# Kernel optimization log

Hardware: AMD Instinct MI355X
Metric: run time of the kernel (lower is better)

## Reference

```python
import jax, jax.numpy as jnp
import numpy as np

OHKM_K = 8
STRUCT_WEIGHT = 1.0
# Standard COCO person skeleton (19 edges over 17 keypoints)
COCO_PERSON_SKELETON = np.array([
    (15, 13), (13, 11), (16, 14), (14, 12), (11, 12), (5, 11), (6, 12),
    (5, 6), (5, 7), (6, 8), (7, 9), (8, 10), (1, 2), (0, 1), (0, 2),
    (1, 3), (2, 4), (3, 5), (4, 6)], dtype=np.int32)


def setup_inputs() -> dict:
    key = jax.random.key(0)
    k1, k2, k3, k4, k5 = jax.random.split(key, 5)
    B, K, C_paf, H, W = 32, 17, 38, 128, 128
    return {
        "heatmap_pred": jax.random.normal(k1, (B, K, H, W), dtype=jnp.float32),
        "paf_pred": jax.random.normal(k2, (B, C_paf, H, W), dtype=jnp.float32),
        "heatmap_gt": jax.random.uniform(k3, (B, K, H, W), dtype=jnp.float32),
        "paf_gt": jax.random.normal(k4, (B, C_paf, H, W), dtype=jnp.float32),
        "joint_coords_gt": jax.random.randint(k5, (B, K, 2), 0, 128, dtype=jnp.int32),
    }


def _struct_loss(heatmap_pred, joint_coords_gt):
    # pred coords from heatmap argmax (vectorized replacement of the python loop)
    B, K, H, W = heatmap_pred.shape
    idx = jnp.argmax(heatmap_pred.reshape(B, K, H * W), axis=2)  # [B,K]
    px = (idx % W).astype(jnp.float32)
    py = (idx // W).astype(jnp.float32)
    pred = jnp.stack([px, py], axis=-1)                 # [B,K,2] (x,y)
    gt = joint_coords_gt.astype(jnp.float32)            # [B,K,2]
    edges = jnp.asarray(COCO_PERSON_SKELETON)           # [E,2]
    a, b = edges[:, 0], edges[:, 1]
    pred_len = jnp.sqrt(jnp.sum((pred[:, a] - pred[:, b]) ** 2, axis=-1))  # [B,E]
    gt_len = jnp.sqrt(jnp.sum((gt[:, a] - gt[:, b]) ** 2, axis=-1))        # [B,E]
    E = edges.shape[0]  # count: all edges valid
    per_batch = jnp.sum((pred_len - gt_len) ** 2, axis=1) / (E + 1e-6)
    return jnp.mean(per_batch)


def reference(heatmap_pred, paf_pred, heatmap_gt, paf_gt, joint_coords_gt):
    # OHKM heatmap loss: per-keypoint MSE, top-k hardest per sample, mean
    per_kp_loss = jnp.mean((heatmap_pred - heatmap_gt) ** 2, axis=(2, 3))  # [B,K]
    Kk = min(OHKM_K, per_kp_loss.shape[1])
    topk_vals, _ = jax.lax.top_k(per_kp_loss, Kk)                          # [B,Kk]
    heatmap_loss = jnp.mean(jnp.mean(topk_vals, axis=1))
    paf_loss = jnp.mean((paf_pred - paf_gt) ** 2)
    total = heatmap_loss + paf_loss
    total = total + STRUCT_WEIGHT * _struct_loss(heatmap_pred, joint_coords_gt)
    return total
```

## Files before the change

kernel.cpp:

```cpp
#include <hip/hip_runtime.h>
#include <math.h>

#define B_ 32
#define K_ 17
#define H_ 128
#define W_ 128
#define HW_ (H_ * W_)
#define C_PAF_ 38
#define NE_ 19
#define HM_TILES (B_ * K_)
#define HM_BLOCKS (HM_TILES * 2)
#define HM_HALF 8192
#define PAF_BLOCKS 2432
#define THREADS 256
#define PAF_N ((size_t)B_ * C_PAF_ * H_ * W_)
#define PAF_N4 (PAF_N / 4)

typedef float fvec4 __attribute__((ext_vector_type(4)));

__constant__ int c_edge_a[NE_] = {15,13,16,14,11, 5, 6, 5, 5, 6, 7, 8, 1, 0, 0, 1, 2, 3, 4};
__constant__ int c_edge_b[NE_] = {13,11,14,12,12,11,12, 6, 7, 8, 9,10, 2, 1, 2, 3, 4, 5, 6};

#define WS_SSQH 0
#define WS_MH   (HM_BLOCKS)
#define WS_MIH  (2 * HM_BLOCKS)
#define WS_PAF  (3 * HM_BLOCKS)

__global__ __launch_bounds__(THREADS, 8) void pose_reduce_kernel(
    const float* __restrict__ hm_pred, const float* __restrict__ hm_gt,
    const float* __restrict__ paf_pred, const float* __restrict__ paf_gt,
    float* __restrict__ ws_f, int* __restrict__ ws_i)
{
    __shared__ float s_val[4];
    __shared__ float s_ssq[4];
    __shared__ int   s_idx[4];

    const int t = threadIdx.x;
    const int bid = blockIdx.x;
    const int wave = t >> 6;
    const int lane = t & 63;

    if (bid < HM_BLOCKS) {
        const int tile = bid >> 1;
        const int half = bid & 1;
        const size_t off = (size_t)tile * HW_ + (size_t)half * HM_HALF;
        const fvec4* __restrict__ p = (const fvec4*)(hm_pred + off);
        const fvec4* __restrict__ g = (const fvec4*)(hm_gt   + off);
        float ssq[2] = {0.0f, 0.0f};
        float m[2] = {-INFINITY, -INFINITY};
        int mi[2] = {0, 0};
        #pragma unroll
        for (int ob = 0; ob < 4; ++ob) {
            const int v0 = t + (ob * 2 + 0) * THREADS;
            const int v1 = t + (ob * 2 + 1) * THREADS;
            const fvec4 a0 = __builtin_nontemporal_load(p + v0);
            const fvec4 b0 = __builtin_nontemporal_load(g + v0);
            const fvec4 a1 = __builtin_nontemporal_load(p + v1);
            const fvec4 b1 = __builtin_nontemporal_load(g + v1);
            {
                const float d0 = a0.x - b0.x, d1 = a0.y - b0.y;
                const float d2 = a0.z - b0.z, d3 = a0.w - b0.w;
                ssq[0] += d0 * d0 + d1 * d1 + d2 * d2 + d3 * d3;
                float m4 = a0.x; int k4 = 0;
                if (a0.y > m4) { m4 = a0.y; k4 = 1; }
                if (a0.z > m4) { m4 = a0.z; k4 = 2; }
                if (a0.w > m4) { m4 = a0.w; k4 = 3; }
                if (m4 > m[0]) { m[0] = m4; mi[0] = 4 * v0 + k4; }
            }
            {
                const float d0 = a1.x - b1.x, d1 = a1.y - b1.y;
                const float d2 = a1.z - b1.z, d3 = a1.w - b1.w;
                ssq[1] += d0 * d0 + d1 * d1 + d2 * d2 + d3 * d3;
                float m4 = a1.x; int k4 = 0;
                if (a1.y > m4) { m4 = a1.y; k4 = 1; }
                if (a1.z > m4) { m4 = a1.z; k4 = 2; }
                if (a1.w > m4) { m4 = a1.w; k4 = 3; }
                if (m4 > m[1]) { m[1] = m4; mi[1] = 4 * v1 + k4; }
            }
        }
        float sT = ssq[0] + ssq[1];
        float M; int MI;
        if (m[1] > m[0] || (m[1] == m[0] && mi[1] < mi[0])) { M = m[1]; MI = mi[1]; }
        else { M = m[0]; MI = mi[0]; }
        #pragma unroll
        for (int off2 = 32; off2 > 0; off2 >>= 1) {
            const float m2  = __shfl_down(M,  off2);
            const int   mi2 = __shfl_down(MI, off2);
            const float s2  = __shfl_down(sT, off2);
            sT += s2;
            if (m2 > M || (m2 == M && mi2 < MI)) { M = m2; MI = mi2; }
        }
        if (lane == 0) { s_val[wave] = M; s_idx[wave] = MI; s_ssq[wave] = sT; }
        __syncthreads();
        if (t == 0) {
            #pragma unroll
            for (int wv = 1; wv < 4; ++wv) {
                sT += s_ssq[wv];
                if (s_val[wv] > M || (s_val[wv] == M && s_idx[wv] < MI)) {
                    M = s_val[wv]; MI = s_idx[wv];
                }
            }
            ws_f[WS_SSQH + bid] = sT;
            ws_f[WS_MH + bid] = M;
            ws_i[WS_MIH + bid] = half * HM_HALF + MI;
        }
    } else {
        const int pb = bid - HM_BLOCKS;
        const fvec4* __restrict__ p = (const fvec4*)paf_pred + (size_t)pb * 2048;
        const fvec4* __restrict__ g = (const fvec4*)paf_gt   + (size_t)pb * 2048;
        float ssq[2] = {0.0f, 0.0f};
        #pragma unroll
        for (int ob = 0; ob < 4; ++ob) {
            const int v0 = t + (ob * 2 + 0) * THREADS;
            const int v1 = t + (ob * 2 + 1) * THREADS;
            const fvec4 a0 = __builtin_nontemporal_load(p + v0);
            const fvec4 b0 = __builtin_nontemporal_load(g + v0);
            const fvec4 a1 = __builtin_nontemporal_load(p + v1);
            const fvec4 b1 = __builtin_nontemporal_load(g + v1);
            {
                const float d0 = a0.x - b0.x, d1 = a0.y - b0.y;
                const float d2 = a0.z - b0.z, d3 = a0.w - b0.w;
                ssq[0] += d0 * d0 + d1 * d1 + d2 * d2 + d3 * d3;
            }
            {
                const float d0 = a1.x - b1.x, d1 = a1.y - b1.y;
                const float d2 = a1.z - b1.z, d3 = a1.w - b1.w;
                ssq[1] += d0 * d0 + d1 * d1 + d2 * d2 + d3 * d3;
            }
        }
        float sT = ssq[0] + ssq[1];
        #pragma unroll
        for (int off2 = 32; off2 > 0; off2 >>= 1) sT += __shfl_down(sT, off2);
        if (lane == 0) s_ssq[wave] = sT;
        __syncthreads();
        if (t == 0) ws_f[WS_PAF + pb] = (s_ssq[0] + s_ssq[1]) + (s_ssq[2] + s_ssq[3]);
    }
}

__global__ __launch_bounds__(THREADS) void pose_final_kernel(
    const float* __restrict__ ws_f, const int* __restrict__ ws_i,
    const int* __restrict__ coords, float* __restrict__ out)
{
    __shared__ float s_p[4];
    const int t = threadIdx.x;
    const int wave = t >> 6;
    const int lane = t & 63;

    float ps = 0.0f;
    for (int i = t; i < PAF_BLOCKS; i += THREADS) ps += ws_f[WS_PAF + i];
    #pragma unroll
    for (int off = 32; off > 0; off >>= 1) ps += __shfl_down(ps, off);
    if (lane == 0) s_p[wave] = ps;
    __syncthreads();

    float val = 0.0f;
    if (t < B_) {
        const int b = t;
        float lk[K_];
        float px[K_], py[K_];
        #pragma unroll
        for (int k = 0; k < K_; ++k) {
            const int j = b * K_ + k;
            const float s0 = ws_f[WS_SSQH + 2 * j], s1 = ws_f[WS_SSQH + 2 * j + 1];
            lk[k] = (s0 + s1) * (1.0f / (float)HW_);
            const float m0 = ws_f[WS_MH + 2 * j], m1 = ws_f[WS_MH + 2 * j + 1];
            const int idx = (m1 > m0) ? ws_i[WS_MIH + 2 * j + 1] : ws_i[WS_MIH + 2 * j];
            px[k] = (float)(idx & (W_ - 1));
            py[k] = (float)(idx >> 7);
        }
        float tsum = 0.0f;
        for (int jj = 0; jj < 8; ++jj) {
            int best = 0; float bv = lk[0];
            for (int k = 1; k < K_; ++k) if (lk[k] > bv) { bv = lk[k]; best = k; }
            tsum += bv;
            lk[best] = -INFINITY;
        }
        float s = 0.0f;
        for (int e = 0; e < NE_; ++e) {
            const int ea = c_edge_a[e], eb = c_edge_b[e];
            const float dx = px[ea] - px[eb];
            const float dy = py[ea] - py[eb];
            const float plen = sqrtf(dx * dx + dy * dy);
            const float gax = (float)coords[(b * K_ + ea) * 2];
            const float gay = (float)coords[(b * K_ + ea) * 2 + 1];
            const float gbx = (float)coords[(b * K_ + eb) * 2];
            const float gby = (float)coords[(b * K_ + eb) * 2 + 1];
            const float gx = gax - gbx, gy = gay - gby;
            const float glen = sqrtf(gx * gx + gy * gy);
            const float d = plen - glen;
            s += d * d;
        }
        val = tsum * (1.0f / 8.0f) + s / (19.0f + 1e-6f);
    }
    #pragma unroll
    for (int off = 16; off > 0; off >>= 1) val += __shfl_down(val, off);
    if (t == 0) {
        const float paf_sum = s_p[0] + s_p[1] + s_p[2] + s_p[3];
        out[0] = val * (1.0f / (float)B_) + paf_sum * (1.0f / (float)PAF_N);
    }
}

extern "C" void kernel_launch(void* const* d_in, const int* in_sizes, int n_in,
                              void* d_out, int out_size, void* d_ws, size_t ws_size,
                              hipStream_t stream) {
    const float* hm_pred  = (const float*)d_in[0];
    const float* paf_pred = (const float*)d_in[1];
    const float* hm_gt    = (const float*)d_in[2];
    const float* paf_gt   = (const float*)d_in[3];
    const int*   coords   = (const int*)d_in[4];
    float* out = (float*)d_out;

    float* ws_f = (float*)d_ws;
    int*   ws_i = (int*)d_ws;

    pose_reduce_kernel<<<HM_BLOCKS + PAF_BLOCKS, THREADS, 0, stream>>>(
        hm_pred, hm_gt, paf_pred, paf_gt, ws_f, ws_i);
    pose_final_kernel<<<1, THREADS, 0, stream>>>(ws_f, ws_i, coords, out);
}
```

Measured before the change: 212.9 us.

## Give each reduce block a full heatmap tile and stage final-kernel data in LDS

Each block in the reduce kernel now processes a whole heatmap tile (and a double-size PAF chunk), which halves the grid to 1760 blocks and removes the per-half max merge and its workspace entries. The final kernel runs with 576 threads that cooperatively load the per-tile losses, argmax coords and GT coords into shared memory. The 32 worker threads then read from LDS instead of doing serial global loads, and the top-k and edge loops are unrolled. The trade-off is fewer blocks in the grid (less parallelism and latency hiding) in exchange for less per-block overhead and a cheaper serial tail.

```diff
diff --git a/kernel.cpp b/kernel.cpp
--- a/kernel.cpp
+++ b/kernel.cpp
@@ -8,11 +8,11 @@
 #define HW_ (H_ * W_)
 #define C_PAF_ 38
 #define NE_ 19
-#define HM_TILES (B_ * K_)
-#define HM_BLOCKS (HM_TILES * 2)
-#define HM_HALF 8192
-#define PAF_BLOCKS 2432
+#define HM_BLOCKS 544
+#define PAF_BLOCKS 1216
+#define GRID (HM_BLOCKS + PAF_BLOCKS)
 #define THREADS 256
+#define FT 576
 #define PAF_N ((size_t)B_ * C_PAF_ * H_ * W_)
 #define PAF_N4 (PAF_N / 4)
 
@@ -21,10 +21,9 @@
 __constant__ int c_edge_a[NE_] = {15,13,16,14,11, 5, 6, 5, 5, 6, 7, 8, 1, 0, 0, 1, 2, 3, 4};
 __constant__ int c_edge_b[NE_] = {13,11,14,12,12,11,12, 6, 7, 8, 9,10, 2, 1, 2, 3, 4, 5, 6};
 
-#define WS_SSQH 0
-#define WS_MH   (HM_BLOCKS)
-#define WS_MIH  (2 * HM_BLOCKS)
-#define WS_PAF  (3 * HM_BLOCKS)
+#define WS_SSQ 0
+#define WS_IDX (HM_BLOCKS)
+#define WS_PAF (2 * HM_BLOCKS)
 
 __global__ __launch_bounds__(THREADS, 8) void pose_reduce_kernel(
     const float* __restrict__ hm_pred, const float* __restrict__ hm_gt,
@@ -41,16 +40,14 @@
     const int lane = t & 63;
 
     if (bid < HM_BLOCKS) {
-        const int tile = bid >> 1;
-        const int half = bid & 1;
-        const size_t off = (size_t)tile * HW_ + (size_t)half * HM_HALF;
+        const size_t off = (size_t)bid * HW_;
         const fvec4* __restrict__ p = (const fvec4*)(hm_pred + off);
         const fvec4* __restrict__ g = (const fvec4*)(hm_gt   + off);
         float ssq[2] = {0.0f, 0.0f};
         float m[2] = {-INFINITY, -INFINITY};
         int mi[2] = {0, 0};
-        #pragma unroll
-        for (int ob = 0; ob < 4; ++ob) {
+        #pragma unroll 4
+        for (int ob = 0; ob < 8; ++ob) {
             const int v0 = t + (ob * 2 + 0) * THREADS;
             const int v1 = t + (ob * 2 + 1) * THREADS;
             const fvec4 a0 = __builtin_nontemporal_load(p + v0);
@@ -100,17 +97,16 @@
                     M = s_val[wv]; MI = s_idx[wv];
                 }
             }
-            ws_f[WS_SSQH + bid] = sT;
-            ws_f[WS_MH + bid] = M;
-            ws_i[WS_MIH + bid] = half * HM_HALF + MI;
+            ws_f[WS_SSQ + bid] = sT;
+            ws_i[WS_IDX + bid] = MI;
         }
     } else {
         const int pb = bid - HM_BLOCKS;
-        const fvec4* __restrict__ p = (const fvec4*)paf_pred + (size_t)pb * 2048;
-        const fvec4* __restrict__ g = (const fvec4*)paf_gt   + (size_t)pb * 2048;
+        const fvec4* __restrict__ p = (const fvec4*)paf_pred + (size_t)pb * 4096;
+        const fvec4* __restrict__ g = (const fvec4*)paf_gt   + (size_t)pb * 4096;
         float ssq[2] = {0.0f, 0.0f};
-        #pragma unroll
-        for (int ob = 0; ob < 4; ++ob) {
+        #pragma unroll 4
+        for (int ob = 0; ob < 8; ++ob) {
             const int v0 = t + (ob * 2 + 0) * THREADS;
             const int v1 = t + (ob * 2 + 1) * THREADS;
             const fvec4 a0 = __builtin_nontemporal_load(p + v0);
@@ -137,55 +133,60 @@
     }
 }
 
-__global__ __launch_bounds__(THREADS) void pose_final_kernel(
+__global__ __launch_bounds__(FT) void pose_final_kernel(
     const float* __restrict__ ws_f, const int* __restrict__ ws_i,
     const int* __restrict__ coords, float* __restrict__ out)
 {
-    __shared__ float s_p[4];
+    __shared__ float s_lk[HM_BLOCKS];
+    __shared__ float s_px[HM_BLOCKS];
+    __shared__ float s_py[HM_BLOCKS];
+    __shared__ float s_gx[HM_BLOCKS];
+    __shared__ float s_gy[HM_BLOCKS];
+    __shared__ float s_p[FT / 64];
+
     const int t = threadIdx.x;
     const int wave = t >> 6;
     const int lane = t & 63;
 
     float ps = 0.0f;
-    for (int i = t; i < PAF_BLOCKS; i += THREADS) ps += ws_f[WS_PAF + i];
+    for (int i = t; i < PAF_BLOCKS; i += FT) ps += ws_f[WS_PAF + i];
     #pragma unroll
     for (int off = 32; off > 0; off >>= 1) ps += __shfl_down(ps, off);
     if (lane == 0) s_p[wave] = ps;
+
+    if (t < HM_BLOCKS) {
+        s_lk[t] = ws_f[WS_SSQ + t] * (1.0f / (float)HW_);
+        const int idx = ws_i[WS_IDX + t];
+        s_px[t] = (float)(idx & (W_ - 1));
+        s_py[t] = (float)(idx >> 7);
+        s_gx[t] = (float)coords[2 * t];
+        s_gy[t] = (float)coords[2 * t + 1];
+    }
     __syncthreads();
 
     float val = 0.0f;
     if (t < B_) {
-        const int b = t;
+        const int base = t * K_;
         float lk[K_];
-        float px[K_], py[K_];
-        #pragma unroll
-        for (int k = 0; k < K_; ++k) {
-            const int j = b * K_ + k;
-            const float s0 = ws_f[WS_SSQH + 2 * j], s1 = ws_f[WS_SSQH + 2 * j + 1];
-            lk[k] = (s0 + s1) * (1.0f / (float)HW_);
-            const float m0 = ws_f[WS_MH + 2 * j], m1 = ws_f[WS_MH + 2 * j + 1];
-            const int idx = (m1 > m0) ? ws_i[WS_MIH + 2 * j + 1] : ws_i[WS_MIH + 2 * j];
-            px[k] = (float)(idx & (W_ - 1));
-            py[k] = (float)(idx >> 7);
-        }
+        #pragma unroll
+        for (int k = 0; k < K_; ++k) lk[k] = s_lk[base + k];
         float tsum = 0.0f;
         for (int jj = 0; jj < 8; ++jj) {
             int best = 0; float bv = lk[0];
+            #pragma unroll
             for (int k = 1; k < K_; ++k) if (lk[k] > bv) { bv = lk[k]; best = k; }
             tsum += bv;
             lk[best] = -INFINITY;
         }
         float s = 0.0f;
+        #pragma unroll
         for (int e = 0; e < NE_; ++e) {
-            const int ea = c_edge_a[e], eb = c_edge_b[e];
-            const float dx = px[ea] - px[eb];
-            const float dy = py[ea] - py[eb];
+            const int ea = base + c_edge_a[e], eb = base + c_edge_b[e];
+            const float dx = s_px[ea] - s_px[eb];
+            const float dy = s_py[ea] - s_py[eb];
             const float plen = sqrtf(dx * dx + dy * dy);
-            const float gax = (float)coords[(b * K_ + ea) * 2];
-            const float gay = (float)coords[(b * K_ + ea) * 2 + 1];
-            const float gbx = (float)coords[(b * K_ + eb) * 2];
-            const float gby = (float)coords[(b * K_ + eb) * 2 + 1];
-            const float gx = gax - gbx, gy = gay - gby;
+            const float gx = s_gx[ea] - s_gx[eb];
+            const float gy = s_gy[ea] - s_gy[eb];
             const float glen = sqrtf(gx * gx + gy * gy);
             const float d = plen - glen;
             s += d * d;
@@ -195,7 +196,9 @@
     #pragma unroll
     for (int off = 16; off > 0; off >>= 1) val += __shfl_down(val, off);
     if (t == 0) {
-        const float paf_sum = s_p[0] + s_p[1] + s_p[2] + s_p[3];
+        float paf_sum = 0.0f;
+        #pragma unroll
+        for (int wv = 0; wv < FT / 64; ++wv) paf_sum += s_p[wv];
         out[0] = val * (1.0f / (float)B_) + paf_sum * (1.0f / (float)PAF_N);
     }
 }
@@ -213,7 +216,7 @@
     float* ws_f = (float*)d_ws;
     int*   ws_i = (int*)d_ws;
 
-    pose_reduce_kernel<<<HM_BLOCKS + PAF_BLOCKS, THREADS, 0, stream>>>(
+    pose_reduce_kernel<<<GRID, THREADS, 0, stream>>>(
         hm_pred, hm_gt, paf_pred, paf_gt, ws_f, ws_i);
-    pose_final_kernel<<<1, THREADS, 0, stream>>>(ws_f, ws_i, coords, out);
+    pose_final_kernel<<<1, FT, 0, stream>>>(ws_f, ws_i, coords, out);
 }
```

New measurement: 210.4 us. No clear change (-1.2%).
